# Performance work log

Hardware: AMD Instinct MI355X
Metric: run time of the kernel (lower is better)

Reference implementation:

```python
import jax, jax.numpy as jnp
import numpy as np

LATENT = 256
HIDDEN = 512
NODE_F = 128
MAX_NODES = 50
B = 128


def _mk_linear(key, fan_in, fan_out):
    kw, kb = jax.random.split(key)
    bound = 1.0 / np.sqrt(fan_in)
    W = jax.random.uniform(kw, (fan_in, fan_out), jnp.float32, -bound, bound)
    b = jax.random.uniform(kb, (fan_out,), jnp.float32, -bound, bound)
    return W, b


def setup_inputs() -> dict:
    key = jax.random.key(0)
    ks = jax.random.split(key, 7)
    z = jax.random.normal(ks[0], (B, LATENT), jnp.float32)
    # node decoder: latent -> hidden -> hidden -> max_nodes*node_features
    nw1, nb1 = _mk_linear(ks[1], LATENT, HIDDEN)
    nw2, nb2 = _mk_linear(ks[2], HIDDEN, HIDDEN)
    nw3, nb3 = _mk_linear(ks[3], HIDDEN, MAX_NODES * NODE_F)
    # edge decoder: latent + 2*node_features -> hidden -> hidden//2 -> 1
    ew1, eb1 = _mk_linear(ks[4], LATENT + 2 * NODE_F, HIDDEN)
    ew2, eb2 = _mk_linear(ks[5], HIDDEN, HIDDEN // 2)
    ew3, eb3 = _mk_linear(ks[6], HIDDEN // 2, 1)
    return {"z": z,
            "nw1": nw1, "nb1": nb1, "nw2": nw2, "nb2": nb2, "nw3": nw3, "nb3": nb3,
            "ew1": ew1, "eb1": eb1, "ew2": ew2, "eb2": eb2, "ew3": ew3, "eb3": eb3}


def reference(z, nw1, nb1, nw2, nb2, nw3, nb3, ew1, eb1, ew2, eb2, ew3, eb3):
    # ---- node decoder ----
    h = jax.nn.relu(z @ nw1 + nb1)
    h = jax.nn.relu(h @ nw2 + nb2)
    node_logits = h @ nw3 + nb3                      # [B, MAX_NODES*NODE_F]
    node_feats = node_logits.reshape(z.shape[0], MAX_NODES, NODE_F)
    node_probs = jax.nn.sigmoid(node_feats)

    # ---- edge decoder: vectorize the O(N^2) python loop over upper-tri pairs ----
    # jnp.triu_indices matches the torch loop order: i ascending, j ascending per i.
    ii, jj = jnp.triu_indices(MAX_NODES, k=1)        # [P] each, P = 1225
    ni = node_feats[:, ii, :]                        # [B, P, NODE_F]
    nj = node_feats[:, jj, :]                        # [B, P, NODE_F]
    zb = jnp.broadcast_to(z[:, None, :], (z.shape[0], ii.shape[0], z.shape[1]))
    edge_in = jnp.concatenate([zb, ni, nj], axis=-1)  # [B, P, LATENT+2*NODE_F]
    e = jax.nn.relu(edge_in @ ew1 + eb1)             # [B, P, HIDDEN]
    e = jax.nn.relu(e @ ew2 + eb2)                   # [B, P, HIDDEN//2]
    edge_probs = jax.nn.sigmoid(e @ ew3 + eb3)[..., 0]  # [B, P]
    return node_probs, edge_probs
```

## Files before the change

kernel.cpp:

```cpp
#include <hip/hip_runtime.h>
#include <math.h>

#define LATENT 256
#define HIDDEN 512
#define NODE_F 128
#define MAX_NODES 50
#define NPAIRS 1225
#define BATCH 128
#define NODE_OUT 6400
#define MTILE 64
#define PTILES 20

typedef __attribute__((ext_vector_type(8))) short short8;
typedef __attribute__((ext_vector_type(4))) float float4v;

__device__ __forceinline__ float bf2f(ushort u) {
    union { unsigned int i; float f; } v; v.i = ((unsigned int)u) << 16; return v.f;
}
__device__ __forceinline__ ushort f2bf(float f) {
    union { unsigned int i; float f; } v; v.f = f;
    unsigned int r = v.i + 0x7fffu + ((v.i >> 16) & 1u);
    return (ushort)(r >> 16);
}
__device__ __forceinline__ float sigmoidf(float x) {
    return 1.0f / (1.0f + __expf(-x));
}

#define TR3_B0   0
#define PREP_B0  800
#define ZC_B0    1824
#define H1_B0    2080
#define PREPK_NB 2336

__global__ __launch_bounds__(256) void k_prep_all(
    const float* __restrict__ nw3, ushort* __restrict__ nw3T,
    const float* __restrict__ ew1, const float* __restrict__ ew2,
    ushort* __restrict__ ew2T, ushort* __restrict__ wijT,
    const float* __restrict__ z, const float* __restrict__ eb1,
    float* __restrict__ Zc,
    const float* __restrict__ nw1, const float* __restrict__ nb1,
    float* __restrict__ h1f)
{
    __shared__ float smem[64 * 65];
    int b = blockIdx.x;
    int tid = threadIdx.x;

    if (b < PREP_B0) {
        int bb = b - TR3_B0;
        int k0 = (bb & 7) * 64;
        int n0 = (bb >> 3) * 64;
        int tx = tid & 63, ty = tid >> 6;
#pragma unroll
        for (int r = 0; r < 16; r++) {
            int row = r * 4 + ty;
            smem[row * 65 + tx] = nw3[(k0 + row) * NODE_OUT + n0 + tx];
        }
        __syncthreads();
#pragma unroll
        for (int c = 0; c < 16; c++) {
            int n = c * 4 + ty;
            nw3T[(size_t)(n0 + n) * HIDDEN + k0 + tx] = f2bf(smem[tx * 65 + n]);
        }
    } else if (b < ZC_B0) {
        int t = (b - PREP_B0) * 256 + tid;
        if (t < 256 * 512) {
            int n = t >> 9, k = t & 511;
            ew2T[t] = f2bf(ew2[k * 256 + n]);
        } else {
            int u = t - 256 * 512;
            int n = u >> 7, k = u & 127;
            float s = (n < 512) ? ew1[(256 + k) * 512 + n] : ew1[(384 + k) * 512 + (n - 512)];
            wijT[u] = f2bf(s);
        }
    } else if (b < H1_B0) {
        int b2 = b - ZC_B0;
        int r = b2 >> 1, o = (b2 & 1) * 256 + tid;
        float* zs = smem;
        zs[tid] = z[r * LATENT + tid];
        __syncthreads();
        float acc = 0.f;
#pragma unroll 8
        for (int k = 0; k < LATENT; k++) acc += zs[k] * ew1[k * HIDDEN + o];
        Zc[r * HIDDEN + o] = acc + eb1[o];
    } else {
        int b2 = b - H1_B0;
        int r = b2 >> 1, o = (b2 & 1) * 256 + tid;
        float* zs = smem;
        zs[tid] = z[r * LATENT + tid];
        __syncthreads();
        float acc = 0.f;
#pragma unroll 8
        for (int k = 0; k < LATENT; k++) acc += zs[k] * nw1[k * HIDDEN + o];
        acc += nb1[o];
        h1f[r * HIDDEN + o] = fmaxf(acc, 0.f);
    }
}

__global__ __launch_bounds__(256) void k_node_h2(
    const float* __restrict__ h1, const float* __restrict__ nw2,
    const float* __restrict__ nb2, ushort* __restrict__ h2b)
{
    __shared__ float hs[HIDDEN];
    int r = blockIdx.x >> 1;
    int o = (blockIdx.x & 1) * 256 + threadIdx.x;
    hs[threadIdx.x] = h1[r * HIDDEN + threadIdx.x];
    hs[threadIdx.x + 256] = h1[r * HIDDEN + threadIdx.x + 256];
    __syncthreads();
    float acc = 0.f;
#pragma unroll 8
    for (int k = 0; k < HIDDEN; k++) acc += hs[k] * nw2[k * HIDDEN + o];
    acc += nb2[o];
    h2b[r * HIDDEN + o] = f2bf(fmaxf(acc, 0.f));
}

__global__ __launch_bounds__(256, 4) void k_node_out_mfma(
    const ushort* __restrict__ h2b, const ushort* __restrict__ nw3T,
    const float* __restrict__ nb3, float* __restrict__ node_probs,
    ushort* __restrict__ node_feats)
{
    int tid = threadIdx.x;
    int wave = tid >> 6, lane = tid & 63;
    int m16 = lane & 15, quad = lane >> 4;
    int n0 = (blockIdx.x >> 2) * 64;
    int m0 = (blockIdx.x & 3) * 32;
    int col = n0 + wave * 16 + m16;

    float4v acc[2];
    acc[0] = (float4v)(0.f); acc[1] = (float4v)(0.f);

    const ushort* bb = nw3T + (size_t)col * HIDDEN;
    const ushort* a0p = h2b + (m0 + m16) * HIDDEN;
    const ushort* a1p = h2b + (m0 + 16 + m16) * HIDDEN;
#pragma unroll
    for (int it = 0; it < 16; ++it) {
        int kk = it * 32 + quad * 8;
        short8 b = *(const short8*)(bb + kk);
        short8 a0 = *(const short8*)(a0p + kk);
        short8 a1 = *(const short8*)(a1p + kk);
        acc[0] = __builtin_amdgcn_mfma_f32_16x16x32_bf16(a0, b, acc[0], 0, 0, 0);
        acc[1] = __builtin_amdgcn_mfma_f32_16x16x32_bf16(a1, b, acc[1], 0, 0, 0);
    }
    float bias = nb3[col];
#pragma unroll
    for (int mt = 0; mt < 2; mt++)
#pragma unroll
        for (int t = 0; t < 4; t++) {
            int row = m0 + mt * 16 + quad * 4 + t;
            float v = acc[mt][t] + bias;
            node_probs[(size_t)row * NODE_OUT + col] = sigmoidf(v);
            node_feats[(size_t)row * NODE_OUT + col] = f2bf(v);
        }
}

__global__ __launch_bounds__(256, 4) void k_uv(
    const ushort* __restrict__ nf, const ushort* __restrict__ wijT,
    ushort* __restrict__ UV)
{
    int tid = threadIdx.x;
    int wave = tid >> 6, lane = tid & 63;
    int m16 = lane & 15, quad = lane >> 4;
    int bm = blockIdx.x >> 2, bn = blockIdx.x & 3;
    int base = bn * 256 + wave * 64;
    int r0 = bm * 64;

    float4v acc[4][4];
#pragma unroll
    for (int mt = 0; mt < 4; mt++)
#pragma unroll
        for (int nt = 0; nt < 4; nt++) acc[mt][nt] = (float4v)(0.f);

#pragma unroll
    for (int k0 = 0; k0 < NODE_F; k0 += 32) {
        int kk = k0 + quad * 8;
        short8 a0 = *(const short8*)(nf + (r0 + m16) * NODE_F + kk);
        short8 a1 = *(const short8*)(nf + (r0 + 16 + m16) * NODE_F + kk);
        short8 a2 = *(const short8*)(nf + (r0 + 32 + m16) * NODE_F + kk);
        short8 a3 = *(const short8*)(nf + (r0 + 48 + m16) * NODE_F + kk);
#pragma unroll
        for (int nt = 0; nt < 4; nt++) {
            int n = base + nt * 16 + m16;
            short8 b = *(const short8*)(wijT + n * NODE_F + kk);
            acc[0][nt] = __builtin_amdgcn_mfma_f32_16x16x32_bf16(a0, b, acc[0][nt], 0, 0, 0);
            acc[1][nt] = __builtin_amdgcn_mfma_f32_16x16x32_bf16(a1, b, acc[1][nt], 0, 0, 0);
            acc[2][nt] = __builtin_amdgcn_mfma_f32_16x16x32_bf16(a2, b, acc[2][nt], 0, 0, 0);
            acc[3][nt] = __builtin_amdgcn_mfma_f32_16x16x32_bf16(a3, b, acc[3][nt], 0, 0, 0);
        }
    }
#pragma unroll
    for (int nt = 0; nt < 4; nt++) {
        int colg = base + nt * 16 + m16;
#pragma unroll
        for (int mt = 0; mt < 4; mt++)
#pragma unroll
            for (int t = 0; t < 4; t++) {
                int rr = r0 + mt * 16 + quad * 4 + t;
                UV[(size_t)rr * 1024 + colg] = f2bf(acc[mt][nt][t]);
            }
    }
}

__global__ __launch_bounds__(512, 4) void k_edge5(
    const float* __restrict__ Zc, const ushort* __restrict__ UV,
    const ushort* __restrict__ ew2T, const float* __restrict__ ew3,
    const float* __restrict__ eb2, const float* __restrict__ eb3,
    float* __restrict__ out_edges)
{
    __shared__ __align__(16) ushort h1[MTILE][HIDDEN + 8];
    __shared__ float part[MTILE][8];
    __shared__ int uo[MTILE], vo[MTILE];

    int blk = blockIdx.x;
    int b   = blk / PTILES;
    int t0  = (blk - b * PTILES) * MTILE;

    int tid = threadIdx.x;
    if (tid < MTILE) {
        int p = t0 + tid;
        if (p >= NPAIRS) p = NPAIRS - 1;
        int i = 0, off = 0;
        while (p - off >= MAX_NODES - 1 - i) { off += MAX_NODES - 1 - i; ++i; }
        int j = i + 1 + (p - off);
        uo[tid] = (b * MAX_NODES + i) * 1024;
        vo[tid] = (b * MAX_NODES + j) * 1024 + 512;
    }

    int wave = tid >> 6, lane = tid & 63;

    int c8 = lane * 8;
    float4v zA = *(const float4v*)(Zc + b * HIDDEN + c8);
    float4v zB = *(const float4v*)(Zc + b * HIDDEN + c8 + 4);
    __syncthreads();

#pragma unroll
    for (int rr = 0; rr < 8; rr++) {
        int r = wave * 8 + rr;
        short8 u8 = *(const short8*)(UV + uo[r] + c8);
        short8 v8 = *(const short8*)(UV + vo[r] + c8);
        short8 hh;
#pragma unroll
        for (int e = 0; e < 8; e++) {
            float zz = (e < 4) ? zA[e] : zB[e - 4];
            hh[e] = (short)f2bf(fmaxf(zz + bf2f((ushort)u8[e]) + bf2f((ushort)v8[e]), 0.f));
        }
        *(short8*)&h1[r][c8] = hh;
    }
    __syncthreads();

    int m16 = lane & 15, quad = lane >> 4;

    float eb2v[2], ew3v[2];
    const ushort* bbase[2];
#pragma unroll
    for (int nt = 0; nt < 2; nt++) {
        int col = wave * 32 + nt * 16 + m16;
        eb2v[nt] = eb2[col];
        ew3v[nt] = ew3[col];
        bbase[nt] = ew2T + col * HIDDEN;
    }

    float4v acc2[4][2];
#pragma unroll
    for (int mt = 0; mt < 4; mt++)
#pragma unroll
        for (int nt = 0; nt < 2; nt++) acc2[mt][nt] = (float4v)(0.f);

    int kk0 = quad * 8;
#pragma unroll
    for (int it = 0; it < 16; ++it) {
        int kk = it * 32 + kk0;
        short8 b0 = *(const short8*)(bbase[0] + kk);
        short8 b1 = *(const short8*)(bbase[1] + kk);
        short8 a0 = *(const short8*)&h1[m16][kk];
        short8 a1 = *(const short8*)&h1[16 + m16][kk];
        short8 a2 = *(const short8*)&h1[32 + m16][kk];
        short8 a3 = *(const short8*)&h1[48 + m16][kk];
        acc2[0][0] = __builtin_amdgcn_mfma_f32_16x16x32_bf16(a0, b0, acc2[0][0], 0, 0, 0);
        acc2[1][0] = __builtin_amdgcn_mfma_f32_16x16x32_bf16(a1, b0, acc2[1][0], 0, 0, 0);
        acc2[2][0] = __builtin_amdgcn_mfma_f32_16x16x32_bf16(a2, b0, acc2[2][0], 0, 0, 0);
        acc2[3][0] = __builtin_amdgcn_mfma_f32_16x16x32_bf16(a3, b0, acc2[3][0], 0, 0, 0);
        acc2[0][1] = __builtin_amdgcn_mfma_f32_16x16x32_bf16(a0, b1, acc2[0][1], 0, 0, 0);
        acc2[1][1] = __builtin_amdgcn_mfma_f32_16x16x32_bf16(a1, b1, acc2[1][1], 0, 0, 0);
        acc2[2][1] = __builtin_amdgcn_mfma_f32_16x16x32_bf16(a2, b1, acc2[2][1], 0, 0, 0);
        acc2[3][1] = __builtin_amdgcn_mfma_f32_16x16x32_bf16(a3, b1, acc2[3][1], 0, 0, 0);
    }

#pragma unroll
    for (int mt = 0; mt < 4; mt++)
#pragma unroll
        for (int t = 0; t < 4; t++) {
            float s = 0.f;
#pragma unroll
            for (int nt = 0; nt < 2; nt++)
                s += fmaxf(acc2[mt][nt][t] + eb2v[nt], 0.f) * ew3v[nt];
            s += __shfl_xor(s, 1);
            s += __shfl_xor(s, 2);
            s += __shfl_xor(s, 4);
            s += __shfl_xor(s, 8);
            if (m16 == 0) part[mt * 16 + quad * 4 + t][wave] = s;
        }
    __syncthreads();

    if (tid < MTILE && t0 + tid < NPAIRS) {
        float v = eb3[0];
#pragma unroll
        for (int w = 0; w < 8; w++) v += part[tid][w];
        out_edges[b * NPAIRS + t0 + tid] = sigmoidf(v);
    }
}

extern "C" void kernel_launch(void* const* d_in, const int* in_sizes, int n_in,
                              void* d_out, int out_size, void* d_ws, size_t ws_size,
                              hipStream_t stream) {
    const float* z   = (const float*)d_in[0];
    const float* nw1 = (const float*)d_in[1];
    const float* nb1 = (const float*)d_in[2];
    const float* nw2 = (const float*)d_in[3];
    const float* nb2 = (const float*)d_in[4];
    const float* nw3 = (const float*)d_in[5];
    const float* nb3 = (const float*)d_in[6];
    const float* ew1 = (const float*)d_in[7];
    const float* eb1 = (const float*)d_in[8];
    const float* ew2 = (const float*)d_in[9];
    const float* eb2 = (const float*)d_in[10];
    const float* ew3 = (const float*)d_in[11];
    const float* eb3 = (const float*)d_in[12];

    char* ws = (char*)d_ws;
    float*  h1f  = (float*)(ws);
    ushort* h2b  = (ushort*)(ws + 262144);
    ushort* nf   = (ushort*)(ws + 393216);
    ushort* ew2T = (ushort*)(ws + 2031616);
    ushort* wijT = (ushort*)(ws + 2293760);
    ushort* nw3T = (ushort*)(ws + 2555904);
    float*  Zc   = (float*)(ws + 9109504);
    ushort* UV   = (ushort*)(ws + 9371648);

    float* out_nodes = (float*)d_out;
    float* out_edges = out_nodes + BATCH * NODE_OUT;

    k_prep_all<<<PREPK_NB, 256, 0, stream>>>(nw3, nw3T, ew1, ew2, ew2T, wijT,
                                             z, eb1, Zc, nw1, nb1, h1f);
    k_node_h2<<<256, 256, 0, stream>>>(h1f, nw2, nb2, h2b);
    k_node_out_mfma<<<400, 256, 0, stream>>>(h2b, nw3T, nb3, out_nodes, nf);
    k_uv<<<400, 256, 0, stream>>>(nf, wijT, UV);
    k_edge5<<<BATCH * PTILES, 512, 0, stream>>>(Zc, UV, ew2T, ew3,
                                                eb2, eb3, out_edges);
}
```

Measured before the change: 248.8 us.

## Fuse node h1/h2 into prep kernel, precompute pair table, prefetch edge operands

Folds the node decoder's second layer into the prep kernel. Each block now recomputes the full h1 row in shared memory and then computes half of h2, which removes one kernel launch and the h1 round trip through global memory at the cost of duplicating the h1 work. A small pair-index table is built once so the edge kernel no longer runs a serial while-loop per pair. The edge kernel also issues all its UV gathers before converting them, and double-buffers the ew2T B-operand loads across the MFMA k-loop, which raises register use.

```diff
diff --git a/kernel.cpp b/kernel.cpp
--- a/kernel.cpp
+++ b/kernel.cpp
@@ -29,8 +29,9 @@
 #define TR3_B0   0
 #define PREP_B0  800
 #define ZC_B0    1824
-#define H1_B0    2080
-#define PREPK_NB 2336
+#define ND_B0    2080
+#define PT_B0    2336
+#define PREPK_NB 2341
 
 __global__ __launch_bounds__(256) void k_prep_all(
     const float* __restrict__ nw3, ushort* __restrict__ nw3T,
@@ -39,7 +40,8 @@
     const float* __restrict__ z, const float* __restrict__ eb1,
     float* __restrict__ Zc,
     const float* __restrict__ nw1, const float* __restrict__ nb1,
-    float* __restrict__ h1f)
+    const float* __restrict__ nw2, const float* __restrict__ nb2,
+    ushort* __restrict__ h2b, int* __restrict__ ptab)
 {
     __shared__ float smem[64 * 65];
     int b = blockIdx.x;
@@ -72,7 +74,7 @@
             float s = (n < 512) ? ew1[(256 + k) * 512 + n] : ew1[(384 + k) * 512 + (n - 512)];
             wijT[u] = f2bf(s);
         }
-    } else if (b < H1_B0) {
+    } else if (b < ND_B0) {
         int b2 = b - ZC_B0;
         int r = b2 >> 1, o = (b2 & 1) * 256 + tid;
         float* zs = smem;
@@ -82,35 +84,38 @@
 #pragma unroll 8
         for (int k = 0; k < LATENT; k++) acc += zs[k] * ew1[k * HIDDEN + o];
         Zc[r * HIDDEN + o] = acc + eb1[o];
-    } else {
-        int b2 = b - H1_B0;
-        int r = b2 >> 1, o = (b2 & 1) * 256 + tid;
+    } else if (b < PT_B0) {
+        int b2 = b - ND_B0;
+        int r = b2 >> 1, half = b2 & 1;
         float* zs = smem;
+        float* hs = smem + 256;
         zs[tid] = z[r * LATENT + tid];
         __syncthreads();
+        float a0 = 0.f, a1 = 0.f;
+#pragma unroll 8
+        for (int k = 0; k < LATENT; k++) {
+            float zk = zs[k];
+            a0 += zk * nw1[k * HIDDEN + tid];
+            a1 += zk * nw1[k * HIDDEN + tid + 256];
+        }
+        hs[tid]       = fmaxf(a0 + nb1[tid], 0.f);
+        hs[tid + 256] = fmaxf(a1 + nb1[tid + 256], 0.f);
+        __syncthreads();
+        int o = half * 256 + tid;
         float acc = 0.f;
 #pragma unroll 8
-        for (int k = 0; k < LATENT; k++) acc += zs[k] * nw1[k * HIDDEN + o];
-        acc += nb1[o];
-        h1f[r * HIDDEN + o] = fmaxf(acc, 0.f);
-    }
-}
-
-__global__ __launch_bounds__(256) void k_node_h2(
-    const float* __restrict__ h1, const float* __restrict__ nw2,
-    const float* __restrict__ nb2, ushort* __restrict__ h2b)
-{
-    __shared__ float hs[HIDDEN];
-    int r = blockIdx.x >> 1;
-    int o = (blockIdx.x & 1) * 256 + threadIdx.x;
-    hs[threadIdx.x] = h1[r * HIDDEN + threadIdx.x];
-    hs[threadIdx.x + 256] = h1[r * HIDDEN + threadIdx.x + 256];
-    __syncthreads();
-    float acc = 0.f;
-#pragma unroll 8
-    for (int k = 0; k < HIDDEN; k++) acc += hs[k] * nw2[k * HIDDEN + o];
-    acc += nb2[o];
-    h2b[r * HIDDEN + o] = f2bf(fmaxf(acc, 0.f));
+        for (int k = 0; k < HIDDEN; k++) acc += hs[k] * nw2[k * HIDDEN + o];
+        acc += nb2[o];
+        h2b[r * HIDDEN + o] = f2bf(fmaxf(acc, 0.f));
+    } else {
+        int p = (b - PT_B0) * 256 + tid;
+        if (p < NPAIRS) {
+            int i = 0, off = 0;
+            while (p - off >= MAX_NODES - 1 - i) { off += MAX_NODES - 1 - i; ++i; }
+            int j = i + 1 + (p - off);
+            ptab[p] = (i << 8) | j;
+        }
+    }
 }
 
 __global__ __launch_bounds__(256, 4) void k_node_out_mfma(
@@ -199,11 +204,11 @@
     }
 }
 
-__global__ __launch_bounds__(512, 4) void k_edge5(
+__global__ __launch_bounds__(512, 4) void k_edge6(
     const float* __restrict__ Zc, const ushort* __restrict__ UV,
     const ushort* __restrict__ ew2T, const float* __restrict__ ew3,
     const float* __restrict__ eb2, const float* __restrict__ eb3,
-    float* __restrict__ out_edges)
+    const int* __restrict__ ptab, float* __restrict__ out_edges)
 {
     __shared__ __align__(16) ushort h1[MTILE][HIDDEN + 8];
     __shared__ float part[MTILE][8];
@@ -217,30 +222,32 @@
     if (tid < MTILE) {
         int p = t0 + tid;
         if (p >= NPAIRS) p = NPAIRS - 1;
-        int i = 0, off = 0;
-        while (p - off >= MAX_NODES - 1 - i) { off += MAX_NODES - 1 - i; ++i; }
-        int j = i + 1 + (p - off);
-        uo[tid] = (b * MAX_NODES + i) * 1024;
-        vo[tid] = (b * MAX_NODES + j) * 1024 + 512;
+        int ij = ptab[p];
+        uo[tid] = (b * MAX_NODES + (ij >> 8)) * 1024;
+        vo[tid] = (b * MAX_NODES + (ij & 255)) * 1024 + 512;
     }
 
     int wave = tid >> 6, lane = tid & 63;
-
     int c8 = lane * 8;
     float4v zA = *(const float4v*)(Zc + b * HIDDEN + c8);
     float4v zB = *(const float4v*)(Zc + b * HIDDEN + c8 + 4);
     __syncthreads();
 
+    short8 uu[8], vv[8];
 #pragma unroll
     for (int rr = 0; rr < 8; rr++) {
         int r = wave * 8 + rr;
-        short8 u8 = *(const short8*)(UV + uo[r] + c8);
-        short8 v8 = *(const short8*)(UV + vo[r] + c8);
+        uu[rr] = *(const short8*)(UV + uo[r] + c8);
+        vv[rr] = *(const short8*)(UV + vo[r] + c8);
+    }
+#pragma unroll
+    for (int rr = 0; rr < 8; rr++) {
+        int r = wave * 8 + rr;
         short8 hh;
 #pragma unroll
         for (int e = 0; e < 8; e++) {
             float zz = (e < 4) ? zA[e] : zB[e - 4];
-            hh[e] = (short)f2bf(fmaxf(zz + bf2f((ushort)u8[e]) + bf2f((ushort)v8[e]), 0.f));
+            hh[e] = (short)f2bf(fmaxf(zz + bf2f((ushort)uu[rr][e]) + bf2f((ushort)vv[rr][e]), 0.f));
         }
         *(short8*)&h1[r][c8] = hh;
     }
@@ -265,23 +272,39 @@
         for (int nt = 0; nt < 2; nt++) acc2[mt][nt] = (float4v)(0.f);
 
     int kk0 = quad * 8;
-#pragma unroll
-    for (int it = 0; it < 16; ++it) {
-        int kk = it * 32 + kk0;
-        short8 b0 = *(const short8*)(bbase[0] + kk);
-        short8 b1 = *(const short8*)(bbase[1] + kk);
-        short8 a0 = *(const short8*)&h1[m16][kk];
-        short8 a1 = *(const short8*)&h1[16 + m16][kk];
-        short8 a2 = *(const short8*)&h1[32 + m16][kk];
-        short8 a3 = *(const short8*)&h1[48 + m16][kk];
-        acc2[0][0] = __builtin_amdgcn_mfma_f32_16x16x32_bf16(a0, b0, acc2[0][0], 0, 0, 0);
-        acc2[1][0] = __builtin_amdgcn_mfma_f32_16x16x32_bf16(a1, b0, acc2[1][0], 0, 0, 0);
-        acc2[2][0] = __builtin_amdgcn_mfma_f32_16x16x32_bf16(a2, b0, acc2[2][0], 0, 0, 0);
-        acc2[3][0] = __builtin_amdgcn_mfma_f32_16x16x32_bf16(a3, b0, acc2[3][0], 0, 0, 0);
-        acc2[0][1] = __builtin_amdgcn_mfma_f32_16x16x32_bf16(a0, b1, acc2[0][1], 0, 0, 0);
-        acc2[1][1] = __builtin_amdgcn_mfma_f32_16x16x32_bf16(a1, b1, acc2[1][1], 0, 0, 0);
-        acc2[2][1] = __builtin_amdgcn_mfma_f32_16x16x32_bf16(a2, b1, acc2[2][1], 0, 0, 0);
-        acc2[3][1] = __builtin_amdgcn_mfma_f32_16x16x32_bf16(a3, b1, acc2[3][1], 0, 0, 0);
+    short8 bp[2][2][2];
+#pragma unroll
+    for (int i = 0; i < 2; i++) {
+        bp[0][i][0] = *(const short8*)(bbase[0] + i * 32 + kk0);
+        bp[0][i][1] = *(const short8*)(bbase[1] + i * 32 + kk0);
+    }
+#pragma unroll
+    for (int g = 0; g < 8; g++) {
+        int cur = g & 1, nxt = cur ^ 1;
+        if (g < 7) {
+#pragma unroll
+            for (int i = 0; i < 2; i++) {
+                int kk = (g + 1) * 64 + i * 32 + kk0;
+                bp[nxt][i][0] = *(const short8*)(bbase[0] + kk);
+                bp[nxt][i][1] = *(const short8*)(bbase[1] + kk);
+            }
+        }
+#pragma unroll
+        for (int i = 0; i < 2; i++) {
+            int kk = g * 64 + i * 32 + kk0;
+            short8 a0 = *(const short8*)&h1[m16][kk];
+            short8 a1 = *(const short8*)&h1[16 + m16][kk];
+            short8 a2 = *(const short8*)&h1[32 + m16][kk];
+            short8 a3 = *(const short8*)&h1[48 + m16][kk];
+            acc2[0][0] = __builtin_amdgcn_mfma_f32_16x16x32_bf16(a0, bp[cur][i][0], acc2[0][0], 0, 0, 0);
+            acc2[1][0] = __builtin_amdgcn_mfma_f32_16x16x32_bf16(a1, bp[cur][i][0], acc2[1][0], 0, 0, 0);
+            acc2[2][0] = __builtin_amdgcn_mfma_f32_16x16x32_bf16(a2, bp[cur][i][0], acc2[2][0], 0, 0, 0);
+            acc2[3][0] = __builtin_amdgcn_mfma_f32_16x16x32_bf16(a3, bp[cur][i][0], acc2[3][0], 0, 0, 0);
+            acc2[0][1] = __builtin_amdgcn_mfma_f32_16x16x32_bf16(a0, bp[cur][i][1], acc2[0][1], 0, 0, 0);
+            acc2[1][1] = __builtin_amdgcn_mfma_f32_16x16x32_bf16(a1, bp[cur][i][1], acc2[1][1], 0, 0, 0);
+            acc2[2][1] = __builtin_amdgcn_mfma_f32_16x16x32_bf16(a2, bp[cur][i][1], acc2[2][1], 0, 0, 0);
+            acc2[3][1] = __builtin_amdgcn_mfma_f32_16x16x32_bf16(a3, bp[cur][i][1], acc2[3][1], 0, 0, 0);
+        }
     }
 
 #pragma unroll
@@ -326,7 +349,7 @@
     const float* eb3 = (const float*)d_in[12];
 
     char* ws = (char*)d_ws;
-    float*  h1f  = (float*)(ws);
+    int*    ptab = (int*)(ws);
     ushort* h2b  = (ushort*)(ws + 262144);
     ushort* nf   = (ushort*)(ws + 393216);
     ushort* ew2T = (ushort*)(ws + 2031616);
@@ -339,10 +362,10 @@
     float* out_edges = out_nodes + BATCH * NODE_OUT;
 
     k_prep_all<<<PREPK_NB, 256, 0, stream>>>(nw3, nw3T, ew1, ew2, ew2T, wijT,
-                                             z, eb1, Zc, nw1, nb1, h1f);
-    k_node_h2<<<256, 256, 0, stream>>>(h1f, nw2, nb2, h2b);
+                                             z, eb1, Zc, nw1, nb1, nw2, nb2,
+                                             h2b, ptab);
     k_node_out_mfma<<<400, 256, 0, stream>>>(h2b, nw3T, nb3, out_nodes, nf);
     k_uv<<<400, 256, 0, stream>>>(nf, wijT, UV);
-    k_edge5<<<BATCH * PTILES, 512, 0, stream>>>(Zc, UV, ew2T, ew3,
-                                                eb2, eb3, out_edges);
-}
+    k_edge6<<<BATCH * PTILES, 512, 0, stream>>>(Zc, UV, ew2T, ew3,
+                                                eb2, eb3, ptab, out_edges);
+}
```

Measured after the change: 243.4 us. 1.02x faster.
